# Optimization experiments

Measured on AMD Instinct MI355X. Metric: run time of the kernel, lower is better.

## Reference

```python
import jax, jax.numpy as jnp
import numpy as np

BS, T, NE, NA, ED = 32, 64, 32, 8, 128
H, A, NH, NACT = 512, 512, 8, 32
HD = A // NH  # 64
SCALE = np.float32(np.sqrt(HD))


def setup_inputs() -> dict:
    key = jax.random.key(0)
    ks = jax.random.split(key, 12)
    inputs = jax.random.normal(ks[0], (BS, T, NE, ED), jnp.float32)
    obs_mask = jax.random.randint(ks[1], (BS, T, NE, NE), 0, 2, jnp.int32)
    scenario_mask = jax.random.randint(ks[2], (BS, T, NE), 0, 2, jnp.int32)
    hidden_state = jnp.zeros((BS * NA, H), jnp.float32)
    g = lambda k, shp: jax.random.normal(k, shp, jnp.float32) * 0.05
    return {
        'inputs': inputs, 'obs_mask': obs_mask, 'scenario_mask': scenario_mask,
        'hidden_state': hidden_state,
        'W1': g(ks[3], (ED, H)), 'b1': jnp.zeros((H,), jnp.float32),
        'Wq': g(ks[4], (H, A)), 'bq': jnp.zeros((A,), jnp.float32),
        'Wk': g(ks[5], (H, A)), 'bk': jnp.zeros((A,), jnp.float32),
        'Wv': g(ks[6], (H, A)), 'bv': jnp.zeros((A,), jnp.float32),
        'Wih': g(ks[7], (3 * H, A)), 'bih': jnp.zeros((3 * H,), jnp.float32),
        'Whh': g(ks[8], (3 * H, H)), 'bhh': jnp.zeros((3 * H,), jnp.float32),
        'Wo': g(ks[9], (H, NACT)), 'bo': jnp.zeros((NACT,), jnp.float32),
    }


def reference(inputs, obs_mask, scenario_mask, hidden_state,
              W1, b1, Wq, bq, Wk, bk, Wv, bv, Wih, bih, Whh, bhh, Wo, bo):
    # fc1: embed every entity  [BS,T,NE,H]
    x = jax.nn.relu(inputs @ W1 + b1)
    q = (x @ Wq + bq).reshape(BS, T, NE, NH, HD)[:, :, :NA]   # agent queries
    k = (x @ Wk + bk).reshape(BS, T, NE, NH, HD)
    v = jax.nn.relu(x @ Wv + bv).reshape(BS, T, NE, NH, HD)
    # scores [BS,T,NH,NA,NE]
    score = jnp.einsum('btqhe,btkhe->bthqk', q, k) / SCALE
    am = obs_mask[:, :, :NA, :].astype(bool)                  # [BS,T,NA,NE]
    score = jnp.where(am[:, :, None], -jnp.inf, score)
    w = jax.nn.softmax(score, axis=-1)
    w = jnp.where(jnp.isnan(w), 0.0, w)                       # fully-masked rows -> 0
    att = jnp.einsum('bthqk,btkhe->btqhe', w, v).reshape(BS, T, NA, A)
    agent_mask = scenario_mask[:, :, :NA].astype(bool)        # [BS,T,NA]
    att = jnp.where(agent_mask[..., None], 0.0, att)
    # per-timestep GRUCell over flattened (BS*NA) rows
    xs = att.transpose(1, 0, 2, 3).reshape(T, BS * NA, A)
    def step(h, xt):
        gi = xt @ Wih.T + bih
        gh = h @ Whh.T + bhh
        ir, iz, inn = jnp.split(gi, 3, axis=-1)
        hr, hz, hn = jnp.split(gh, 3, axis=-1)
        r = jax.nn.sigmoid(ir + hr)
        z = jax.nn.sigmoid(iz + hz)
        n = jnp.tanh(inn + r * hn)
        hn_ = (1.0 - z) * n + z * h
        return hn_, hn_
    _, hs = jax.lax.scan(step, hidden_state, xs)              # [T,BS*NA,H]
    hs = hs.reshape(T, BS, NA, H).transpose(1, 0, 2, 3)       # [BS,T,NA,H]
    qout = hs @ Wo + bo                                       # [BS,T,NA,NACT]
    hs = jnp.where(agent_mask[..., None], 0.0, hs)
    qout = jnp.where(agent_mask[..., None], 0.0, qout)
    return qout, hs
```

## Files before the change

### kernel.cpp

```cpp
#include <hip/hip_runtime.h>
#include <hip/hip_bf16.h>
#include <cstddef>
#include <cstdint>

typedef __hip_bfloat16 bf16;
typedef __attribute__((ext_vector_type(2))) _Float16 half2v;
typedef __attribute__((ext_vector_type(8))) _Float16 half8;
typedef __attribute__((ext_vector_type(8))) short short8;
typedef __attribute__((ext_vector_type(4))) float f32x4;
typedef __attribute__((ext_vector_type(2))) unsigned long long u64x2;

__device__ inline float ldf(const float* p) { return *p; }
__device__ inline float ldf(const bf16* p) { return __bfloat162float(*p); }
__device__ inline void stf(float* p, float v) { *p = v; }
__device__ inline void stf(bf16* p, float v) { *p = __float2bfloat16(v); }
__device__ inline short bfb(float v) { return __builtin_bit_cast(short, __float2bfloat16(v)); }

__device__ inline half8 h8_from(unsigned long long lo, unsigned long long hi) {
    u64x2 t; t.x = lo; t.y = hi;
    return __builtin_bit_cast(half8, t);
}
__device__ inline float fsig(float x) {
    x = fminf(fmaxf(x, -60.f), 60.f);
    return 1.f / (1.f + __expf(-x));
}
__device__ inline float ftanh(float x) {
    x = fminf(fmaxf(x, -15.f), 15.f);
    float e = __expf(2.f * x);
    return 1.f - 2.f / (e + 1.f);
}
__device__ inline void unpack8(uint4 u, float4& lo, float4& hi) {
    uint32_t w0 = u.x, w1 = u.y, w2 = u.z, w3 = u.w;
    lo.x = __builtin_bit_cast(float, (w0 & 0xffffu) << 16);
    lo.y = __builtin_bit_cast(float, w0 & 0xffff0000u);
    lo.z = __builtin_bit_cast(float, (w1 & 0xffffu) << 16);
    lo.w = __builtin_bit_cast(float, w1 & 0xffff0000u);
    hi.x = __builtin_bit_cast(float, (w2 & 0xffffu) << 16);
    hi.y = __builtin_bit_cast(float, w2 & 0xffff0000u);
    hi.z = __builtin_bit_cast(float, (w3 & 0xffffu) << 16);
    hi.w = __builtin_bit_cast(float, w3 & 0xffff0000u);
}
__device__ inline uint32_t pk2(float a, float b) {
    return ((uint32_t)(uint16_t)bfb(a)) | (((uint32_t)(uint16_t)bfb(b)) << 16);
}


template<int ACT, bool QG, typename TA, typename TC>
__global__ __launch_bounds__(256) void mfma_gemm_k(
    const TA* __restrict__ A, const bf16* __restrict__ Bt,
    const float* __restrict__ bias, TC* __restrict__ C,
    int M, int N, int K)
{
    __shared__ short As[2][4096];
    __shared__ short Bs[2][4096];
    const int tid = threadIdx.x;
    const int lane = tid & 63, wid = tid >> 6;
    const int wm = wid >> 1, wn = wid & 1;
    const int bm = blockIdx.y * 128, bn = blockIdx.x * 128;
    const int fr = lane & 15, fq = lane >> 4;

    f32x4 acc[4][4] = {};

    auto stage = [&](int buf, int k0) {
#if __has_builtin(__builtin_amdgcn_global_load_lds)
        #pragma unroll
        for (int j = 0; j < 2; ++j) {
            int jj = wid * 2 + j;
            int row = jj * 16 + (lane >> 2);
            const short* src = (const short*)Bt + (size_t)(bn + row) * K + k0 + (lane & 3) * 8;
            __builtin_amdgcn_global_load_lds(
                (const __attribute__((address_space(1))) void*)src,
                (__attribute__((address_space(3))) void*)&Bs[buf][jj * 512], 16, 0, 0);
        }
        if constexpr (sizeof(TA) == 2) {
            #pragma unroll
            for (int j = 0; j < 2; ++j) {
                int jj = wid * 2 + j;
                int row = jj * 16 + (lane >> 2);
                int gm = bm + row;
                int ar = QG ? (((gm >> 3) << 5) | (gm & 7)) : gm;
                const short* src = (const short*)A + (size_t)ar * K + k0 + (lane & 3) * 8;
                __builtin_amdgcn_global_load_lds(
                    (const __attribute__((address_space(1))) void*)src,
                    (__attribute__((address_space(3))) void*)&As[buf][jj * 512], 16, 0, 0);
            }
        } else {
            int sr = tid >> 1, sk = (tid & 1) * 16;
            int gm = bm + sr;
            int ar = QG ? (((gm >> 3) << 5) | (gm & 7)) : gm;
            const float* ap = (const float*)A + (size_t)ar * K + k0 + sk;
            float4 f0 = *(const float4*)(ap);
            float4 f1 = *(const float4*)(ap + 4);
            float4 f2 = *(const float4*)(ap + 8);
            float4 f3 = *(const float4*)(ap + 12);
            short tmp[16] = {bfb(f0.x), bfb(f0.y), bfb(f0.z), bfb(f0.w),
                             bfb(f1.x), bfb(f1.y), bfb(f1.z), bfb(f1.w),
                             bfb(f2.x), bfb(f2.y), bfb(f2.z), bfb(f2.w),
                             bfb(f3.x), bfb(f3.y), bfb(f3.z), bfb(f3.w)};
            *(uint4*)&As[buf][sr * 32 + sk]     = *(const uint4*)&tmp[0];
            *(uint4*)&As[buf][sr * 32 + sk + 8] = *(const uint4*)&tmp[8];
        }
#else
        {
            int sr = tid >> 1, sk = (tid & 1) * 16;
            int gm = bm + sr;
            int ar = QG ? (((gm >> 3) << 5) | (gm & 7)) : gm;
            if constexpr (sizeof(TA) == 4) {
                const float* ap = (const float*)A + (size_t)ar * K + k0 + sk;
                short tmp[16];
                #pragma unroll
                for (int j = 0; j < 16; ++j) tmp[j] = bfb(ap[j]);
                *(uint4*)&As[buf][sr * 32 + sk]     = *(const uint4*)&tmp[0];
                *(uint4*)&As[buf][sr * 32 + sk + 8] = *(const uint4*)&tmp[8];
            } else {
                const short* ap = (const short*)A + (size_t)ar * K + k0 + sk;
                *(uint4*)&As[buf][sr * 32 + sk]     = *(const uint4*)(ap);
                *(uint4*)&As[buf][sr * 32 + sk + 8] = *(const uint4*)(ap + 8);
            }
            const short* bp = (const short*)Bt + (size_t)(bn + sr) * K + k0 + sk;
            *(uint4*)&Bs[buf][sr * 32 + sk]     = *(const uint4*)(bp);
            *(uint4*)&Bs[buf][sr * 32 + sk + 8] = *(const uint4*)(bp + 8);
        }
#endif
    };

    const int nt = K >> 5;
    stage(0, 0);
    __syncthreads();

    for (int t = 0; t < nt; ++t) {
        int cur = t & 1;
        if (t + 1 < nt) stage(cur ^ 1, (t + 1) * 32);

        short8 af[4], bg[4];
        #pragma unroll
        for (int m = 0; m < 4; ++m)
            af[m] = *(const short8*)&As[cur][(wm * 64 + m * 16 + fr) * 32 + fq * 8];
        #pragma unroll
        for (int n = 0; n < 4; ++n)
            bg[n] = *(const short8*)&Bs[cur][(wn * 64 + n * 16 + fr) * 32 + fq * 8];
        #pragma unroll
        for (int m = 0; m < 4; ++m)
            #pragma unroll
            for (int n = 0; n < 4; ++n)
                acc[m][n] = __builtin_amdgcn_mfma_f32_16x16x32_bf16(
                    af[m], bg[n], acc[m][n], 0, 0, 0);
        __syncthreads();
    }

    #pragma unroll
    for (int m = 0; m < 4; ++m) {
        #pragma unroll
        for (int n = 0; n < 4; ++n) {
            int col = bn + wn * 64 + n * 16 + fr;
            float bv = bias[col];
            #pragma unroll
            for (int r = 0; r < 4; ++r) {
                int row = bm + wm * 64 + m * 16 + fq * 4 + r;
                float v = acc[m][n][r] + bv;
                if (ACT == 1) v = fmaxf(v, 0.f);
                if (ACT == 2 && col >= 512) v = fmaxf(v, 0.f);
                stf(&C[(size_t)row * N + col], v);
            }
        }
    }
}

__global__ __launch_bounds__(256) void prep_all_k(
    const float* __restrict__ W1, const float* __restrict__ Wq,
    const float* __restrict__ Wk, const float* __restrict__ Wv,
    const float* __restrict__ Wo, const float* __restrict__ h0,
    const float* __restrict__ bk, const float* __restrict__ bv,
    bf16* __restrict__ W1t, bf16* __restrict__ Wqt, bf16* __restrict__ Wkvt,
    bf16* __restrict__ Wot, _Float16* __restrict__ ha, float* __restrict__ bkv)
{
    int blk = blockIdx.x;
    int tid = threadIdx.x;
    if (blk < 848) {
        const float* src; bf16* dst; int K, N, ti;
        if (blk < 64)       { src = W1; dst = W1t;  K = 128; N = 512; ti = blk; }
        else if (blk < 320) { src = Wq; dst = Wqt;  K = 512; N = 512; ti = blk - 64; }
        else if (blk < 576) { src = Wk; dst = Wkvt; K = 512; N = 512; ti = blk - 320; }
        else if (blk < 832) { src = Wv; dst = Wkvt + 512 * 512; K = 512; N = 512; ti = blk - 576; }
        else                { src = Wo; dst = Wot;  K = 512; N = 32;  ti = blk - 832; }
        int kt = K >> 5;
        int tk = ti % kt, tn = ti / kt;
        int k0 = tk * 32, n0 = tn * 32;
        __shared__ float tile[32][33];
        int tx = tid & 31, ty = tid >> 5;
        #pragma unroll
        for (int i = 0; i < 4; ++i) {
            int r = ty + i * 8;
            tile[r][tx] = src[(size_t)(k0 + r) * N + n0 + tx];
        }
        __syncthreads();
        #pragma unroll
        for (int i = 0; i < 4; ++i) {
            int r = ty + i * 8;
            if (n0 + r < N)
                dst[(size_t)(n0 + r) * K + k0 + tx] = __float2bfloat16(tile[tx][r]);
        }
        return;
    }
    int idx = (blk - 848) * 256 + tid;
    if (idx < 131072) { ha[idx] = (_Float16)h0[idx]; return; }
    idx -= 131072;
    if (idx < 1024) { bkv[idx] = (idx < 512) ? bk[idx] : bv[idx - 512]; return; }
}

__global__ __launch_bounds__(256) void qout_mfma_k(
    const float* __restrict__ hs, const bf16* __restrict__ Wot,
    const float* __restrict__ bo, const int* __restrict__ smask,
    float* __restrict__ out)
{
    __shared__ short Bs2[32 * 520];
    __shared__ short As2[128 * 32];
    const int tid = threadIdx.x;
    const int lane = tid & 63, wid = tid >> 6;
    const int bm = blockIdx.x * 128;
    const int fr = lane & 15, fq = lane >> 4;

    for (int i = tid; i < 2048; i += 256) {
        int row = i >> 6, col = (i & 63) * 8;
        *(uint4*)&Bs2[row * 520 + col] = *(const uint4*)((const short*)Wot + row * 512 + col);
    }

    f32x4 acc[2][2] = {};
    for (int k0 = 0; k0 < 512; k0 += 32) {
        {
            int sr = tid >> 1, sk = (tid & 1) * 16;
            const float* ap = hs + (size_t)(bm + sr) * 512 + k0 + sk;
            float4 f0 = *(const float4*)(ap);
            float4 f1 = *(const float4*)(ap + 4);
            float4 f2 = *(const float4*)(ap + 8);
            float4 f3 = *(const float4*)(ap + 12);
            short tmp[16] = {bfb(f0.x), bfb(f0.y), bfb(f0.z), bfb(f0.w),
                             bfb(f1.x), bfb(f1.y), bfb(f1.z), bfb(f1.w),
                             bfb(f2.x), bfb(f2.y), bfb(f2.z), bfb(f2.w),
                             bfb(f3.x), bfb(f3.y), bfb(f3.z), bfb(f3.w)};
            *(uint4*)&As2[sr * 32 + sk]     = *(const uint4*)&tmp[0];
            *(uint4*)&As2[sr * 32 + sk + 8] = *(const uint4*)&tmp[8];
        }
        __syncthreads();
        short8 af[2], bg[2];
        #pragma unroll
        for (int m = 0; m < 2; ++m)
            af[m] = *(const short8*)&As2[(wid * 32 + m * 16 + fr) * 32 + fq * 8];
        #pragma unroll
        for (int n = 0; n < 2; ++n)
            bg[n] = *(const short8*)&Bs2[(n * 16 + fr) * 520 + k0 + fq * 8];
        #pragma unroll
        for (int m = 0; m < 2; ++m)
            #pragma unroll
            for (int n = 0; n < 2; ++n)
                acc[m][n] = __builtin_amdgcn_mfma_f32_16x16x32_bf16(
                    af[m], bg[n], acc[m][n], 0, 0, 0);
        __syncthreads();
    }

    #pragma unroll
    for (int m = 0; m < 2; ++m) {
        #pragma unroll
        for (int n = 0; n < 2; ++n) {
            int col = n * 16 + fr;
            float bv = bo[col];
            #pragma unroll
            for (int r = 0; r < 4; ++r) {
                int row = bm + wid * 32 + m * 16 + fq * 4 + r;
                int a_ = row & 7, t_ = (row >> 3) & 63, b_ = row >> 9;
                bool mz = smask[((b_ << 6) + t_) * 32 + a_] != 0;
                out[(size_t)row * 32 + col] = mz ? 0.f : (acc[m][n][r] + bv);
            }
        }
    }
}

#define AST 68
__global__ __launch_bounds__(64) void attn_k(
    const bf16* __restrict__ qb, const bf16* __restrict__ kb, const bf16* __restrict__ vb,
    const int* __restrict__ obs, const int* __restrict__ smask, bf16* __restrict__ xs,
    int kvstride)
{
    __shared__ float qs[8 * AST], ks[32 * AST], vs[32 * AST], wsm[8 * 33];
    int bid = blockIdx.x;
    int h = bid & 7;
    int bt = bid >> 3;
    int t = bt & 63, b = bt >> 6;
    int tid = threadIdx.x;

    {
        int srow = tid >> 3, c0 = (tid & 7) * 8;
        float4 lo, hi;
        uint4 qv = *(const uint4*)&qb[((size_t)bt * 8 + srow) * 512 + h * 64 + c0];
        unpack8(qv, lo, hi);
        *(float4*)&qs[srow * AST + c0] = lo;
        *(float4*)&qs[srow * AST + c0 + 4] = hi;
        #pragma unroll
        for (int i = 0; i < 4; ++i) {
            int row = srow + i * 8;
            uint4 kv4 = *(const uint4*)&kb[((size_t)bt * 32 + row) * kvstride + h * 64 + c0];
            unpack8(kv4, lo, hi);
            *(float4*)&ks[row * AST + c0] = lo;
            *(float4*)&ks[row * AST + c0 + 4] = hi;
            uint4 vv4 = *(const uint4*)&vb[((size_t)bt * 32 + row) * kvstride + h * 64 + c0];
            unpack8(vv4, lo, hi);
            *(float4*)&vs[row * AST + c0] = lo;
            *(float4*)&vs[row * AST + c0 + 4] = hi;
        }
    }
    __syncthreads();

    int ql = tid >> 3, jl = tid & 7;
    float s[4];
    #pragma unroll
    for (int c = 0; c < 4; ++c) {
        int kl = jl + c * 8;
        float4 a4 = make_float4(0.f, 0.f, 0.f, 0.f);
        #pragma unroll 4
        for (int d4 = 0; d4 < 16; ++d4) {
            float4 q4 = *(const float4*)&qs[ql * AST + d4 * 4];
            float4 k4 = *(const float4*)&ks[kl * AST + d4 * 4];
            a4.x += q4.x * k4.x; a4.y += q4.y * k4.y;
            a4.z += q4.z * k4.z; a4.w += q4.w * k4.w;
        }
        float acc = (a4.x + a4.y) + (a4.z + a4.w);
        acc *= 0.125f;
        bool m = obs[(((size_t)bt * 32) + ql) * 32 + kl] != 0;
        s[c] = m ? -__builtin_inff() : acc;
    }
    float mx = fmaxf(fmaxf(s[0], s[1]), fmaxf(s[2], s[3]));
    for (int off = 1; off < 8; off <<= 1) mx = fmaxf(mx, __shfl_xor(mx, off));
    float e4[4]; float sum = 0.f;
    bool allmasked = (mx == -__builtin_inff());
    #pragma unroll
    for (int c = 0; c < 4; ++c) {
        e4[c] = (allmasked || s[c] == -__builtin_inff()) ? 0.f : expf(s[c] - mx);
        sum += e4[c];
    }
    for (int off = 1; off < 8; off <<= 1) sum += __shfl_xor(sum, off);
    float inv = (sum > 0.f) ? 1.f / sum : 0.f;
    #pragma unroll
    for (int c = 0; c < 4; ++c) wsm[ql * 33 + jl + c * 8] = e4[c] * inv;
    __syncthreads();

    bool amask = smask[(size_t)bt * 32 + ql] != 0;
    int d0 = jl * 8;
    float4 o0 = make_float4(0.f, 0.f, 0.f, 0.f);
    float4 o1 = make_float4(0.f, 0.f, 0.f, 0.f);
    #pragma unroll 4
    for (int kl = 0; kl < 32; ++kl) {
        float w = wsm[ql * 33 + kl];
        float4 v0 = *(const float4*)&vs[kl * AST + d0];
        float4 v1 = *(const float4*)&vs[kl * AST + d0 + 4];
        o0.x += w * v0.x; o0.y += w * v0.y; o0.z += w * v0.z; o0.w += w * v0.w;
        o1.x += w * v1.x; o1.y += w * v1.y; o1.z += w * v1.z; o1.w += w * v1.w;
    }
    if (amask) { o0 = make_float4(0.f, 0.f, 0.f, 0.f); o1 = o0; }
    uint4 pk;
    pk.x = pk2(o0.x, o0.y); pk.y = pk2(o0.z, o0.w);
    pk.z = pk2(o1.x, o1.y); pk.w = pk2(o1.z, o1.w);
    *(uint4*)&xs[((size_t)(t * 256 + b * 8 + ql)) * 512 + h * 64 + d0] = pk;
}

__global__ __launch_bounds__(128, 1) void gru_xcd_k(
    const bf16* __restrict__ xs, const float* __restrict__ Wih,
    const float* __restrict__ bih,
    const float* __restrict__ Whh, const float* __restrict__ bhh,
    const float* __restrict__ h0,
    const int* __restrict__ smask, float* __restrict__ hs_out,
    _Float16* __restrict__ ha, _Float16* __restrict__ hb, int* __restrict__ flags)
{
    __shared__ _Float16 wh16[48 * 520];
    __shared__ short    wi16[48 * 520];
    const int tid = threadIdx.x;
    const int lane = tid & 63, wid = tid >> 6;
    const int g = blockIdx.x;
    const int grp = g & 7, cu = g >> 3;
    const int r0 = grp * 32;
    const int hc0 = cu * 16;
    const int fr = lane & 15, fq = lane >> 4;
    const int hcol = hc0 + fr;
    const int rw0 = r0 + wid * 16;
    const int row0 = rw0 + fq * 4;

    for (int i = tid; i < 6144; i += 128) {
        int flat = i * 4;
        int r = flat >> 9, c = flat & 511;
        int wr = (r >> 4) * 512 + hc0 + (r & 15);
        float4 v = *(const float4*)(Whh + (size_t)wr * 512 + c);
        half2v p0; p0[0] = (_Float16)v.x; p0[1] = (_Float16)v.y;
        half2v p1; p1[0] = (_Float16)v.z; p1[1] = (_Float16)v.w;
        *(uint32_t*)&wh16[r * 520 + c]     = __builtin_bit_cast(uint32_t, p0);
        *(uint32_t*)&wh16[r * 520 + c + 2] = __builtin_bit_cast(uint32_t, p1);
        float4 u = *(const float4*)(Wih + (size_t)wr * 512 + c);
        uint32_t w0 = (uint32_t)(uint16_t)bfb(u.x) | ((uint32_t)(uint16_t)bfb(u.y) << 16);
        uint32_t w1 = (uint32_t)(uint16_t)bfb(u.z) | ((uint32_t)(uint16_t)bfb(u.w) << 16);
        *(uint32_t*)&wi16[r * 520 + c]     = w0;
        *(uint32_t*)&wi16[r * 520 + c + 2] = w1;
    }

    const float bhr = bhh[hcol], bhz = bhh[512 + hcol], bhn = bhh[1024 + hcol];
    const float bir = bih[hcol], biz = bih[512 + hcol], bin_ = bih[1024 + hcol];

    float hp[4];
    #pragma unroll
    for (int r = 0; r < 4; ++r)
        hp[r] = h0[(size_t)(row0 + r) * 512 + hcol];

    __syncthreads();

    f32x4 gcur[3] = {};
    int mcur[4];
    {
        const short* xp = (const short*)xs + ((size_t)0 * 256 + rw0 + fr) * 512 + fq * 8;
        short8 ax[16];
        #pragma unroll
        for (int ks = 0; ks < 16; ++ks) ax[ks] = *(const short8*)(xp + ks * 32);
        #pragma unroll
        for (int ks = 0; ks < 16; ++ks) {
            const short* bb = &wi16[fr * 520 + ks * 32 + fq * 8];
            short8 b0 = *(const short8*)(bb);
            short8 b1 = *(const short8*)(bb + 16 * 520);
            short8 b2 = *(const short8*)(bb + 32 * 520);
            gcur[0] = __builtin_amdgcn_mfma_f32_16x16x32_bf16(ax[ks], b0, gcur[0], 0, 0, 0);
            gcur[1] = __builtin_amdgcn_mfma_f32_16x16x32_bf16(ax[ks], b1, gcur[1], 0, 0, 0);
            gcur[2] = __builtin_amdgcn_mfma_f32_16x16x32_bf16(ax[ks], b2, gcur[2], 0, 0, 0);
        }
        #pragma unroll
        for (int r = 0; r < 4; ++r) {
            int row = row0 + r;
            mcur[r] = smask[(((row >> 3) << 6) + 0) * 32 + (row & 7)];
        }
    }

    for (int t = 0; t < 64; ++t) {
        const _Float16* hsrc = (t & 1) ? hb : ha;
        _Float16*       hdst = (t & 1) ? ha : hb;

        half8 aA[16];
        {
            const unsigned long long* ap = (const unsigned long long*)
                (hsrc + (size_t)(rw0 + fr) * 512 + fq * 8);
            #pragma unroll
            for (int ks = 0; ks < 16; ++ks) {
                unsigned long long lo = __hip_atomic_load(ap + ks * 8,
                    __ATOMIC_RELAXED, __HIP_MEMORY_SCOPE_AGENT);
                unsigned long long hi = __hip_atomic_load(ap + ks * 8 + 1,
                    __ATOMIC_RELAXED, __HIP_MEMORY_SCOPE_AGENT);
                aA[ks] = h8_from(lo, hi);
            }
        }

        f32x4 acc[3] = {};
        #pragma unroll
        for (int ks = 0; ks < 16; ++ks) {
            const _Float16* bbase = &wh16[fr * 520 + ks * 32 + fq * 8];
            half8 b0 = *(const half8*)(bbase);
            half8 b1 = *(const half8*)(bbase + 16 * 520);
            half8 b2 = *(const half8*)(bbase + 32 * 520);
            acc[0] = __builtin_amdgcn_mfma_f32_16x16x32_f16(aA[ks], b0, acc[0], 0, 0, 0);
            acc[1] = __builtin_amdgcn_mfma_f32_16x16x32_f16(aA[ks], b1, acc[1], 0, 0, 0);
            acc[2] = __builtin_amdgcn_mfma_f32_16x16x32_f16(aA[ks], b2, acc[2], 0, 0, 0);
        }

        float hnv[4];
        #pragma unroll
        for (int r = 0; r < 4; ++r) {
            float rg = fsig(gcur[0][r] + bir + acc[0][r] + bhr);
            float zg = fsig(gcur[1][r] + biz + acc[1][r] + bhz);
            float ng = ftanh(gcur[2][r] + bin_ + rg * (acc[2][r] + bhn));
            float hn = (1.f - zg) * ng + zg * hp[r];
            hp[r] = hn;
            hnv[r] = hn;
            unsigned short hbits = __builtin_bit_cast(unsigned short, (_Float16)hn);
            __hip_atomic_store((unsigned short*)(hdst + (size_t)(row0 + r) * 512 + hcol),
                               hbits, __ATOMIC_RELAXED, __HIP_MEMORY_SCOPE_AGENT);
        }

        if (t != 63) {
            asm volatile("s_waitcnt vmcnt(0)" ::: "memory");
            __builtin_amdgcn_sched_barrier(0);
            if (lane == 0)
                __hip_atomic_store(flags + ((size_t)grp * 64 + t) * 64 + cu * 2 + wid, 1,
                                   __ATOMIC_RELAXED, __HIP_MEMORY_SCOPE_AGENT);
            #pragma unroll
            for (int r = 0; r < 4; ++r) {
                int row = row0 + r;
                int b_ = row >> 3, a_ = row & 7;
                hs_out[((size_t)((b_ << 6) + t) * 8 + a_) * 512 + hcol] =
                    mcur[r] ? 0.f : hnv[r];
            }
            f32x4 gnx[3] = {};
            {
                const short* xp = (const short*)xs +
                    ((size_t)(t + 1) * 256 + rw0 + fr) * 512 + fq * 8;
                short8 ax[16];
                #pragma unroll
                for (int ks = 0; ks < 16; ++ks) ax[ks] = *(const short8*)(xp + ks * 32);
                #pragma unroll
                for (int ks = 0; ks < 16; ++ks) {
                    const short* bb = &wi16[fr * 520 + ks * 32 + fq * 8];
                    short8 b0 = *(const short8*)(bb);
                    short8 b1 = *(const short8*)(bb + 16 * 520);
                    short8 b2 = *(const short8*)(bb + 32 * 520);
                    gnx[0] = __builtin_amdgcn_mfma_f32_16x16x32_bf16(ax[ks], b0, gnx[0], 0, 0, 0);
                    gnx[1] = __builtin_amdgcn_mfma_f32_16x16x32_bf16(ax[ks], b1, gnx[1], 0, 0, 0);
                    gnx[2] = __builtin_amdgcn_mfma_f32_16x16x32_bf16(ax[ks], b2, gnx[2], 0, 0, 0);
                }
            }
            int mnx[4];
            #pragma unroll
            for (int r = 0; r < 4; ++r) {
                int row = row0 + r;
                mnx[r] = smask[(((row >> 3) << 6) + (t + 1)) * 32 + (row & 7)];
            }
            const int* fp = flags + ((size_t)grp * 64 + t) * 64 + lane;
            long it = 0;
            for (;;) {
                int f = __hip_atomic_load(fp, __ATOMIC_RELAXED, __HIP_MEMORY_SCOPE_AGENT);
                if (__all(f != 0) || it > 100000000L) break;
                __builtin_amdgcn_s_sleep(1);
                ++it;
            }
            __builtin_amdgcn_sched_barrier(0);
            gcur[0] = gnx[0]; gcur[1] = gnx[1]; gcur[2] = gnx[2];
            mcur[0] = mnx[0]; mcur[1] = mnx[1]; mcur[2] = mnx[2]; mcur[3] = mnx[3];
        } else {
            #pragma unroll
            for (int r = 0; r < 4; ++r) {
                int row = row0 + r;
                int b_ = row >> 3, a_ = row & 7;
                hs_out[((size_t)((b_ << 6) + t) * 8 + a_) * 512 + hcol] =
                    mcur[r] ? 0.f : hnv[r];
            }
        }
    }
}

extern "C" void kernel_launch(void* const* d_in, const int* in_sizes, int n_in,
                              void* d_out, int out_size, void* d_ws, size_t ws_size,
                              hipStream_t stream)
{
    const float* inputs = (const float*)d_in[0];
    const int*   obs    = (const int*)d_in[1];
    const int*   smask  = (const int*)d_in[2];
    const float* h0     = (const float*)d_in[3];
    const float* W1  = (const float*)d_in[4];  const float* b1  = (const float*)d_in[5];
    const float* Wq  = (const float*)d_in[6];  const float* bq  = (const float*)d_in[7];
    const float* Wk  = (const float*)d_in[8];  const float* bk  = (const float*)d_in[9];
    const float* Wv  = (const float*)d_in[10]; const float* bv  = (const float*)d_in[11];
    const float* Wih = (const float*)d_in[12]; const float* bih = (const float*)d_in[13];
    const float* Whh = (const float*)d_in[14]; const float* bhh = (const float*)d_in[15];
    const float* Wo  = (const float*)d_in[16]; const float* bo  = (const float*)d_in[17];

    char* ws = (char*)d_ws;
    bf16*  x    = (bf16*)(ws + 0);
    bf16*  xs   = (bf16*)(ws + 0);
    bf16*  qb   = (bf16*)(ws + 67108864ull);
    bf16*  kv   = (bf16*)(ws + 83886080ull);
    bf16*  W1t  = (bf16*)(ws + 218103808ull);
    bf16*  Wqt  = (bf16*)(ws + 218234880ull);
    bf16*  Wkvt = (bf16*)(ws + 218759168ull);
    _Float16* ha = (_Float16*)(ws + 219807744ull);
    _Float16* hb = (_Float16*)(ws + 220069888ull);
    int*   flags = (int*)(ws + 220332032ull);
    float* bkv  = (float*)(ws + 220463104ull);
    bf16*  Wot  = (bf16*)(ws + 220467200ull);

    float* out    = (float*)d_out;
    float* hs_out = out + 524288;

    hipMemsetAsync(flags, 0, 131072, stream);

    prep_all_k<<<dim3(1365), 256, 0, stream>>>(
        W1, Wq, Wk, Wv, Wo, h0, bk, bv, W1t, Wqt, Wkvt, Wot, ha, bkv);
    mfma_gemm_k<1, false, float, bf16><<<dim3(4, 512), 256, 0, stream>>>(
        inputs, W1t, b1, x, 65536, 512, 128);
    mfma_gemm_k<0, true, bf16, bf16><<<dim3(4, 128), 256, 0, stream>>>(
        x, Wqt, bq, qb, 16384, 512, 512);
    mfma_gemm_k<2, false, bf16, bf16><<<dim3(8, 512), 256, 0, stream>>>(
        x, Wkvt, bkv, kv, 65536, 1024, 512);
    attn_k<<<dim3(16384), 64, 0, stream>>>(qb, kv, kv + 512, obs, smask, xs, 1024);
    gru_xcd_k<<<dim3(256), 128, 0, stream>>>(
        xs, Wih, bih, Whh, bhh, h0, smask, hs_out, ha, hb, flags);
    qout_mfma_k<<<dim3(128), 256, 0, stream>>>(hs_out, Wot, bo, smask, out);
}
```

Before: 542.3 us.

## Warp-specialize GRU: producer waves compute input gates into LDS double buffer

```diff
diff --git a/kernel.cpp b/kernel.cpp
--- a/kernel.cpp
+++ b/kernel.cpp
@@ -362,7 +362,7 @@
     *(uint4*)&xs[((size_t)(t * 256 + b * 8 + ql)) * 512 + h * 64 + d0] = pk;
 }
 
-__global__ __launch_bounds__(128, 1) void gru_xcd_k(
+__global__ __launch_bounds__(256, 1) void gru_xcd_k(
     const bf16* __restrict__ xs, const float* __restrict__ Wih,
     const float* __restrict__ bih,
     const float* __restrict__ Whh, const float* __restrict__ bhh,
@@ -372,6 +372,7 @@
 {
     __shared__ _Float16 wh16[48 * 520];
     __shared__ short    wi16[48 * 520];
+    __shared__ float    gbuf[2][32][49];
     const int tid = threadIdx.x;
     const int lane = tid & 63, wid = tid >> 6;
     const int g = blockIdx.x;
@@ -380,10 +381,8 @@
     const int hc0 = cu * 16;
     const int fr = lane & 15, fq = lane >> 4;
     const int hcol = hc0 + fr;
-    const int rw0 = r0 + wid * 16;
-    const int row0 = rw0 + fq * 4;
-
-    for (int i = tid; i < 6144; i += 128) {
+
+    for (int i = tid; i < 6144; i += 256) {
         int flat = i * 4;
         int r = flat >> 9, c = flat & 511;
         int wr = (r >> 4) * 512 + hc0 + (r & 15);
@@ -398,91 +397,109 @@
         *(uint32_t*)&wi16[r * 520 + c]     = w0;
         *(uint32_t*)&wi16[r * 520 + c + 2] = w1;
     }
-
-    const float bhr = bhh[hcol], bhz = bhh[512 + hcol], bhn = bhh[1024 + hcol];
-    const float bir = bih[hcol], biz = bih[512 + hcol], bin_ = bih[1024 + hcol];
-
-    float hp[4];
-    #pragma unroll
-    for (int r = 0; r < 4; ++r)
-        hp[r] = h0[(size_t)(row0 + r) * 512 + hcol];
-
     __syncthreads();
 
-    f32x4 gcur[3] = {};
-    int mcur[4];
-    {
-        const short* xp = (const short*)xs + ((size_t)0 * 256 + rw0 + fr) * 512 + fq * 8;
+    auto gi_pass = [&](int tt, int buf) {
+        const int wrow = (wid - 2) * 16;
+        const short* xp = (const short*)xs + ((size_t)tt * 256 + r0 + wrow + fr) * 512 + fq * 8;
         short8 ax[16];
         #pragma unroll
         for (int ks = 0; ks < 16; ++ks) ax[ks] = *(const short8*)(xp + ks * 32);
+        f32x4 gg[3] = {};
         #pragma unroll
         for (int ks = 0; ks < 16; ++ks) {
             const short* bb = &wi16[fr * 520 + ks * 32 + fq * 8];
             short8 b0 = *(const short8*)(bb);
             short8 b1 = *(const short8*)(bb + 16 * 520);
             short8 b2 = *(const short8*)(bb + 32 * 520);
-            gcur[0] = __builtin_amdgcn_mfma_f32_16x16x32_bf16(ax[ks], b0, gcur[0], 0, 0, 0);
-            gcur[1] = __builtin_amdgcn_mfma_f32_16x16x32_bf16(ax[ks], b1, gcur[1], 0, 0, 0);
-            gcur[2] = __builtin_amdgcn_mfma_f32_16x16x32_bf16(ax[ks], b2, gcur[2], 0, 0, 0);
-        }
+            gg[0] = __builtin_amdgcn_mfma_f32_16x16x32_bf16(ax[ks], b0, gg[0], 0, 0, 0);
+            gg[1] = __builtin_amdgcn_mfma_f32_16x16x32_bf16(ax[ks], b1, gg[1], 0, 0, 0);
+            gg[2] = __builtin_amdgcn_mfma_f32_16x16x32_bf16(ax[ks], b2, gg[2], 0, 0, 0);
+        }
+        #pragma unroll
+        for (int gg_i = 0; gg_i < 3; ++gg_i)
+            #pragma unroll
+            for (int r = 0; r < 4; ++r)
+                gbuf[buf][wrow + fq * 4 + r][gg_i * 16 + fr] = gg[gg_i][r];
+    };
+
+    const int rw0 = r0 + (wid & 1) * 16;
+    const int row0 = rw0 + fq * 4;
+    const int lrow = (wid & 1) * 16 + fq * 4;
+    float bhr = 0, bhz = 0, bhn = 0, bir = 0, biz = 0, bin_ = 0;
+    float hp[4];
+    int mcur[4];
+    if (wid < 2) {
+        bhr = bhh[hcol]; bhz = bhh[512 + hcol]; bhn = bhh[1024 + hcol];
+        bir = bih[hcol]; biz = bih[512 + hcol]; bin_ = bih[1024 + hcol];
+        #pragma unroll
+        for (int r = 0; r < 4; ++r)
+            hp[r] = h0[(size_t)(row0 + r) * 512 + hcol];
         #pragma unroll
         for (int r = 0; r < 4; ++r) {
             int row = row0 + r;
             mcur[r] = smask[(((row >> 3) << 6) + 0) * 32 + (row & 7)];
         }
-    }
+    } else {
+        gi_pass(0, 0);
+    }
+    __syncthreads();
 
     for (int t = 0; t < 64; ++t) {
-        const _Float16* hsrc = (t & 1) ? hb : ha;
-        _Float16*       hdst = (t & 1) ? ha : hb;
-
-        half8 aA[16];
-        {
-            const unsigned long long* ap = (const unsigned long long*)
-                (hsrc + (size_t)(rw0 + fr) * 512 + fq * 8);
+        if (wid < 2) {
+            const _Float16* hsrc = (t & 1) ? hb : ha;
+            _Float16*       hdst = (t & 1) ? ha : hb;
+
+            half8 aA[16];
+            {
+                const unsigned long long* ap = (const unsigned long long*)
+                    (hsrc + (size_t)(rw0 + fr) * 512 + fq * 8);
+                #pragma unroll
+                for (int ks = 0; ks < 16; ++ks) {
+                    unsigned long long lo = __hip_atomic_load(ap + ks * 8,
+                        __ATOMIC_RELAXED, __HIP_MEMORY_SCOPE_AGENT);
+                    unsigned long long hi = __hip_atomic_load(ap + ks * 8 + 1,
+                        __ATOMIC_RELAXED, __HIP_MEMORY_SCOPE_AGENT);
+                    aA[ks] = h8_from(lo, hi);
+                }
+            }
+
+            f32x4 acc[3] = {};
             #pragma unroll
             for (int ks = 0; ks < 16; ++ks) {
-                unsigned long long lo = __hip_atomic_load(ap + ks * 8,
-                    __ATOMIC_RELAXED, __HIP_MEMORY_SCOPE_AGENT);
-                unsigned long long hi = __hip_atomic_load(ap + ks * 8 + 1,
-                    __ATOMIC_RELAXED, __HIP_MEMORY_SCOPE_AGENT);
-                aA[ks] = h8_from(lo, hi);
-            }
-        }
-
-        f32x4 acc[3] = {};
-        #pragma unroll
-        for (int ks = 0; ks < 16; ++ks) {
-            const _Float16* bbase = &wh16[fr * 520 + ks * 32 + fq * 8];
-            half8 b0 = *(const half8*)(bbase);
-            half8 b1 = *(const half8*)(bbase + 16 * 520);
-            half8 b2 = *(const half8*)(bbase + 32 * 520);
-            acc[0] = __builtin_amdgcn_mfma_f32_16x16x32_f16(aA[ks], b0, acc[0], 0, 0, 0);
-            acc[1] = __builtin_amdgcn_mfma_f32_16x16x32_f16(aA[ks], b1, acc[1], 0, 0, 0);
-            acc[2] = __builtin_amdgcn_mfma_f32_16x16x32_f16(aA[ks], b2, acc[2], 0, 0, 0);
-        }
-
-        float hnv[4];
-        #pragma unroll
-        for (int r = 0; r < 4; ++r) {
-            float rg = fsig(gcur[0][r] + bir + acc[0][r] + bhr);
-            float zg = fsig(gcur[1][r] + biz + acc[1][r] + bhz);
-            float ng = ftanh(gcur[2][r] + bin_ + rg * (acc[2][r] + bhn));
-            float hn = (1.f - zg) * ng + zg * hp[r];
-            hp[r] = hn;
-            hnv[r] = hn;
-            unsigned short hbits = __builtin_bit_cast(unsigned short, (_Float16)hn);
-            __hip_atomic_store((unsigned short*)(hdst + (size_t)(row0 + r) * 512 + hcol),
-                               hbits, __ATOMIC_RELAXED, __HIP_MEMORY_SCOPE_AGENT);
-        }
-
-        if (t != 63) {
-            asm volatile("s_waitcnt vmcnt(0)" ::: "memory");
-            __builtin_amdgcn_sched_barrier(0);
-            if (lane == 0)
-                __hip_atomic_store(flags + ((size_t)grp * 64 + t) * 64 + cu * 2 + wid, 1,
-                                   __ATOMIC_RELAXED, __HIP_MEMORY_SCOPE_AGENT);
+                const _Float16* bbase = &wh16[fr * 520 + ks * 32 + fq * 8];
+                half8 b0 = *(const half8*)(bbase);
+                half8 b1 = *(const half8*)(bbase + 16 * 520);
+                half8 b2 = *(const half8*)(bbase + 32 * 520);
+                acc[0] = __builtin_amdgcn_mfma_f32_16x16x32_f16(aA[ks], b0, acc[0], 0, 0, 0);
+                acc[1] = __builtin_amdgcn_mfma_f32_16x16x32_f16(aA[ks], b1, acc[1], 0, 0, 0);
+                acc[2] = __builtin_amdgcn_mfma_f32_16x16x32_f16(aA[ks], b2, acc[2], 0, 0, 0);
+            }
+
+            float hnv[4];
+            #pragma unroll
+            for (int r = 0; r < 4; ++r) {
+                float gr_ = gbuf[t & 1][lrow + r][fr];
+                float gz_ = gbuf[t & 1][lrow + r][16 + fr];
+                float gn_ = gbuf[t & 1][lrow + r][32 + fr];
+                float rg = fsig(gr_ + bir + acc[0][r] + bhr);
+                float zg = fsig(gz_ + biz + acc[1][r] + bhz);
+                float ng = ftanh(gn_ + bin_ + rg * (acc[2][r] + bhn));
+                float hn = (1.f - zg) * ng + zg * hp[r];
+                hp[r] = hn;
+                hnv[r] = hn;
+                unsigned short hbits = __builtin_bit_cast(unsigned short, (_Float16)hn);
+                __hip_atomic_store((unsigned short*)(hdst + (size_t)(row0 + r) * 512 + hcol),
+                                   hbits, __ATOMIC_RELAXED, __HIP_MEMORY_SCOPE_AGENT);
+            }
+
+            if (t != 63) {
+                asm volatile("s_waitcnt vmcnt(0)" ::: "memory");
+                __builtin_amdgcn_sched_barrier(0);
+                if (lane == 0)
+                    __hip_atomic_store(flags + ((size_t)grp * 64 + t) * 64 + cu * 2 + wid, 1,
+                                       __ATOMIC_RELAXED, __HIP_MEMORY_SCOPE_AGENT);
+            }
             #pragma unroll
             for (int r = 0; r < 4; ++r) {
                 int row = row0 + r;
@@ -490,30 +507,20 @@
                 hs_out[((size_t)((b_ << 6) + t) * 8 + a_) * 512 + hcol] =
                     mcur[r] ? 0.f : hnv[r];
             }
-            f32x4 gnx[3] = {};
-            {
-                const short* xp = (const short*)xs +
-                    ((size_t)(t + 1) * 256 + rw0 + fr) * 512 + fq * 8;
-                short8 ax[16];
+            if (t != 63) {
                 #pragma unroll
-                for (int ks = 0; ks < 16; ++ks) ax[ks] = *(const short8*)(xp + ks * 32);
-                #pragma unroll
-                for (int ks = 0; ks < 16; ++ks) {
-                    const short* bb = &wi16[fr * 520 + ks * 32 + fq * 8];
-                    short8 b0 = *(const short8*)(bb);
-                    short8 b1 = *(const short8*)(bb + 16 * 520);
-                    short8 b2 = *(const short8*)(bb + 32 * 520);
-                    gnx[0] = __builtin_amdgcn_mfma_f32_16x16x32_bf16(ax[ks], b0, gnx[0], 0, 0, 0);
-                    gnx[1] = __builtin_amdgcn_mfma_f32_16x16x32_bf16(ax[ks], b1, gnx[1], 0, 0, 0);
-                    gnx[2] = __builtin_amdgcn_mfma_f32_16x16x32_bf16(ax[ks], b2, gnx[2], 0, 0, 0);
+                for (int r = 0; r < 4; ++r) {
+                    int row = row0 + r;
+                    mcur[r] = smask[(((row >> 3) << 6) + (t + 1)) * 32 + (row & 7)];
                 }
             }
-            int mnx[4];
-            #pragma unroll
-            for (int r = 0; r < 4; ++r) {
-                int row = row0 + r;
-                mnx[r] = smask[(((row >> 3) << 6) + (t + 1)) * 32 + (row & 7)];
-            }
+        } else {
+            if (t < 63) gi_pass(t + 1, (t + 1) & 1);
+        }
+
+        __syncthreads();
+
+        if (wid < 2 && t != 63) {
             const int* fp = flags + ((size_t)grp * 64 + t) * 64 + lane;
             long it = 0;
             for (;;) {
@@ -523,16 +530,6 @@
                 ++it;
             }
             __builtin_amdgcn_sched_barrier(0);
-            gcur[0] = gnx[0]; gcur[1] = gnx[1]; gcur[2] = gnx[2];
-            mcur[0] = mnx[0]; mcur[1] = mnx[1]; mcur[2] = mnx[2]; mcur[3] = mnx[3];
-        } else {
-            #pragma unroll
-            for (int r = 0; r < 4; ++r) {
-                int row = row0 + r;
-                int b_ = row >> 3, a_ = row & 7;
-                hs_out[((size_t)((b_ << 6) + t) * 8 + a_) * 512 + hcol] =
-                    mcur[r] ? 0.f : hnv[r];
-            }
         }
     }
 }
@@ -581,7 +578,7 @@
     mfma_gemm_k<2, false, bf16, bf16><<<dim3(8, 512), 256, 0, stream>>>(
         x, Wkvt, bkv, kv, 65536, 1024, 512);
     attn_k<<<dim3(16384), 64, 0, stream>>>(qb, kv, kv + 512, obs, smask, xs, 1024);
-    gru_xcd_k<<<dim3(256), 128, 0, stream>>>(
+    gru_xcd_k<<<dim3(256), 256, 0, stream>>>(
         xs, Wih, bih, Whh, bhh, h0, smask, hs_out, ha, hb, flags);
     qout_mfma_k<<<dim3(128), 256, 0, stream>>>(hs_out, Wot, bo, smask, out);
 }
```

Measured after the change: 555.5 us. 1.02x slower.
